# Kernel optimization log

Measured on AMD Instinct MI355X. Metric: run time of the kernel, lower is better.

Reference implementation:

```python
import jax, jax.numpy as jnp
import numpy as np

VERY_SMOL_NUM = -1e9  # undefined global in source; interpreted as large negative mask value
D_K = 128


def setup_inputs() -> dict:
    key = jax.random.key(0)
    k1, k2, k3 = jax.random.split(key, 3)
    B, S, D = 16, 2048, D_K
    Q = jax.random.normal(k1, (B, S, D), dtype=jnp.float32)
    K = jax.random.normal(k2, (B, S, D), dtype=jnp.float32)
    V = jax.random.normal(k3, (B, S, D), dtype=jnp.float32)
    return {"Q": Q, "K": K, "V": V}


def reference(Q, K, V):
    B, S, d_k = Q.shape
    # scores: [B, S, S] = Q @ K^T, scaled by 1/sqrt(d_k)
    x = jnp.einsum("bqd,bkd->bqk", Q, K) / jnp.sqrt(jnp.asarray(d_k, Q.dtype))
    # mask() is called unconditionally in the source (masked=False -> applied once):
    # add strict upper-triangular VERY_SMOL_NUM
    tri = jnp.triu(jnp.ones((S, S), dtype=x.dtype), k=1) * jnp.asarray(VERY_SMOL_NUM, x.dtype)
    x = x + tri  # broadcasts over batch, matching torch.triu on full shape
    # Softmax over dim=1 (query axis), as in the source (torch.nn.Softmax(dim=1))
    x = jax.nn.softmax(x, axis=1)
    return jnp.einsum("bqk,bkd->bqd", x, V)
```

## Files before the change

kernel.cpp:

```cpp
#include <hip/hip_runtime.h>


#define B_ 16
#define S_ 2048
#define D_ 128
#define QSCALE 0.12751744416825963f
#define NEG_BIG -1e30f
#define NCH 16
#define CHQ 128
#define PB 2162688

#define ROWW 136
#define P2RW 24

#define LDS_BARRIER()                                  \
  do {                                                 \
    asm volatile("s_waitcnt lgkmcnt(0)" ::: "memory"); \
    __builtin_amdgcn_s_barrier();                      \
  } while (0)

typedef short bf16x8 __attribute__((ext_vector_type(8)));
typedef float f32x4 __attribute__((ext_vector_type(4)));
typedef unsigned short u16x4 __attribute__((ext_vector_type(4)));
typedef unsigned int u32x2 __attribute__((ext_vector_type(2)));

#if defined(__has_builtin)
#if __has_builtin(__builtin_amdgcn_exp2f)
#define EXP2F(x) __builtin_amdgcn_exp2f(x)
#endif
#endif
#ifndef EXP2F
extern "C" __device__ float __ocml_exp2_f32(float);
#define EXP2F(x) __ocml_exp2_f32(x)
#endif

static __device__ __forceinline__ unsigned short f2bf(float f) {
  unsigned int u = __builtin_bit_cast(unsigned int, f);
  u += 0x7FFFu + ((u >> 16) & 1u);
  return (unsigned short)(u >> 16);
}

__global__ __launch_bounds__(256) void sdpa_convert(
    const float* __restrict__ Qr, const float* __restrict__ Kr,
    unsigned short* __restrict__ Qb, unsigned short* __restrict__ Kb) {
  const size_t t = (size_t)blockIdx.x * 256 + threadIdx.x;
  const float* src = blockIdx.y ? Kr : Qr;
  unsigned short* dstp = blockIdx.y ? Kb : Qb;
  const float sc = blockIdx.y ? 1.0f : QSCALE;
  f32x4 x = ((const f32x4*)src)[t];
  u16x4 o;
#pragma unroll
  for (int j = 0; j < 4; ++j) o[j] = f2bf(x[j] * sc);
  ((u16x4*)dstp)[t] = o;
}

__global__ __launch_bounds__(256, 4) void sdpa_pass1(
    const short* __restrict__ Qb, const short* __restrict__ Kb,
    float* __restrict__ lp_ws, unsigned short* __restrict__ Pt) {
  const int bid = blockIdx.x;
  int j = bid >> 4;
  int g = 0;
  while (j >= NCH - g) {
    j -= NCH - g;
    ++g;
  }
  const int ci = g + j;
  const int b = (bid & 7) + 8 * ((bid >> 3) & 1);

  __shared__ __align__(16) short Qst[2][32 * ROWW];
  const int tid = threadIdx.x;
  const int w = tid >> 6, lane = tid & 63, quad = lane >> 4, l15 = lane & 15;
  const int gg = 2 * g + (w >> 1);
  const int gb = 64 * gg;
  const int kb = gb + (w & 1) * 32;

  const size_t koff = ((size_t)b * S_ + kb + l15) * D_ + quad * 8;
  bf16x8 kh0[4], kh1[4];
#pragma unroll
  for (int c = 0; c < 4; ++c) {
    kh0[c] = *(const bf16x8*)(Kb + koff + c * 32);
    kh1[c] = *(const bf16x8*)(Kb + koff + 16 * D_ + c * 32);
  }

  const int nrp = S_ - gb;
  const size_t grp =
      (size_t)4 * ((size_t)gg * S_ - (size_t)(32 * gg) * (gg - 1));
  unsigned short* pw0 = Pt + (size_t)b * PB +
                        16 * (grp + (size_t)(2 * (w & 1)) * nrp) + quad * 4;
  unsigned short* pw1 = pw0 + (size_t)16 * nrp;

  const int sr = tid >> 3, sseg = tid & 7;
  const int q_start = CHQ * ci;

  {
    const short* sq = Qb + ((size_t)(b * S_ + q_start + sr)) * D_ + sseg * 16;
    bf16x8 h0 = *(const bf16x8*)(sq), h1 = *(const bf16x8*)(sq + 8);
    short* dst = &Qst[0][sr * ROWW + sseg * 16];
    *(bf16x8*)(dst) = h0;
    *(bf16x8*)(dst + 8) = h1;
  }
  LDS_BARRIER();

#define EMIT(q0s_, ktb_, cA_, pw_, lp_)                                       \
  do {                                                                        \
    float s0_ = cA_[0], s1_ = cA_[1], s2_ = cA_[2], s3_ = cA_[3];             \
    if ((q0s_) < (ktb_) + 16) {              \
      const int q_ = (q0s_) + l15;                                            \
      if ((ktb_) + quad * 4 + 0 > q_) s0_ = NEG_BIG;                          \
      if ((ktb_) + quad * 4 + 1 > q_) s1_ = NEG_BIG;                          \
      if ((ktb_) + quad * 4 + 2 > q_) s2_ = NEG_BIG;                          \
      if ((ktb_) + quad * 4 + 3 > q_) s3_ = NEG_BIG;                          \
    }                                                                         \
    const float e0_ = EXP2F(s0_), e1_ = EXP2F(s1_);                           \
    const float e2_ = EXP2F(s2_), e3_ = EXP2F(s3_);                           \
    lp_[0] += e0_;                                                            \
    lp_[1] += e1_;                                                            \
    lp_[2] += e2_;                                                            \
    lp_[3] += e3_;                                                            \
    unsigned int w0_, w1_;                                                    \
    asm("v_cvt_pk_bf16_f32 %0, %1, %2" : "=v"(w0_) : "v"(e0_), "v"(e1_));     \
    asm("v_cvt_pk_bf16_f32 %0, %1, %2" : "=v"(w1_) : "v"(e2_), "v"(e3_));     \
    u32x2 pk2_ = {w0_, w1_};                                                  \
    *(u32x2*)((pw_) + (size_t)((q0s_)-gb + l15) * 16) = pk2_;                 \
  } while (0)

  f32x4 lp0 = {0.f, 0.f, 0.f, 0.f}, lp1 = {0.f, 0.f, 0.f, 0.f};
#pragma unroll
  for (int it = 0; it < 4; ++it) {
    const int q0 = q_start + it * 32;
    const int cur = it & 1;
    bf16x8 h0, h1;
    if (it < 3) {
      const short* sq =
          Qb + ((size_t)(b * S_ + q0 + 32 + sr)) * D_ + sseg * 16;
      h0 = *(const bf16x8*)(sq);
      h1 = *(const bf16x8*)(sq + 8);
    }
#pragma unroll
    for (int sub = 0; sub < 2; ++sub) {
      const int q0s = q0 + sub * 16;
      if (q0s >= gb) {
        const short* rowp = &Qst[cur][(sub * 16 + l15) * ROWW + quad * 8];
        bf16x8 q0v = *(const bf16x8*)(rowp);
        bf16x8 q1v = *(const bf16x8*)(rowp + 32);
        bf16x8 q2v = *(const bf16x8*)(rowp + 64);
        bf16x8 q3v = *(const bf16x8*)(rowp + 96);
        f32x4 c0 = {0.f, 0.f, 0.f, 0.f};
        f32x4 c1 = {0.f, 0.f, 0.f, 0.f};
        c0 = __builtin_amdgcn_mfma_f32_16x16x32_bf16(kh0[0], q0v, c0, 0, 0, 0);
        c1 = __builtin_amdgcn_mfma_f32_16x16x32_bf16(kh1[0], q0v, c1, 0, 0, 0);
        c0 = __builtin_amdgcn_mfma_f32_16x16x32_bf16(kh0[1], q1v, c0, 0, 0, 0);
        c1 = __builtin_amdgcn_mfma_f32_16x16x32_bf16(kh1[1], q1v, c1, 0, 0, 0);
        c0 = __builtin_amdgcn_mfma_f32_16x16x32_bf16(kh0[2], q2v, c0, 0, 0, 0);
        c1 = __builtin_amdgcn_mfma_f32_16x16x32_bf16(kh1[2], q2v, c1, 0, 0, 0);
        c0 = __builtin_amdgcn_mfma_f32_16x16x32_bf16(kh0[3], q3v, c0, 0, 0, 0);
        c1 = __builtin_amdgcn_mfma_f32_16x16x32_bf16(kh1[3], q3v, c1, 0, 0, 0);
        EMIT(q0s, kb, c0, pw0, lp0);
        EMIT(q0s, kb + 16, c1, pw1, lp1);
      }
    }
    if (it < 3) {
      short* dst = &Qst[1 - cur][sr * ROWW + sseg * 16];
      *(bf16x8*)(dst) = h0;
      *(bf16x8*)(dst + 8) = h1;
    }
    LDS_BARRIER();
  }
#undef EMIT

#pragma unroll
  for (int d = 1; d < 16; d <<= 1) {
#pragma unroll
    for (int r = 0; r < 4; ++r) {
      lp0[r] += __shfl_xor(lp0[r], d, 64);
      lp1[r] += __shfl_xor(lp1[r], d, 64);
    }
  }
  if (l15 == 0) {
    float* dst = lp_ws + ((size_t)b * NCH + ci) * S_ + kb;
    *(f32x4*)(dst + quad * 4) = lp0;
    *(f32x4*)(dst + 16 + quad * 4) = lp1;
  }
}

__global__ __launch_bounds__(256) void sdpa_vscale(
    const float* __restrict__ Vr, const float* __restrict__ lp_ws,
    unsigned short* __restrict__ Vf) {
  __shared__ float Vld[32][132];
  __shared__ float as[32];
  const int kt = blockIdx.x, b = blockIdx.y, tid = threadIdx.x;
  const int k0 = kt * 32;
  const int row = tid >> 3, seg = tid & 7;
  const float* src = Vr + ((size_t)(b * S_ + k0 + row)) * D_ + seg * 16;
#pragma unroll
  for (int j = 0; j < 4; ++j) {
    f32x4 x = *(const f32x4*)(src + 4 * j);
    *(f32x4*)&Vld[row][seg * 16 + 4 * j] = x;
  }
  if (tid < 32) {
    const int k = k0 + tid;
    const int first = k >> 7;
    float l = 0.f;
#pragma unroll
    for (int ci = 0; ci < NCH; ++ci)
      if (ci >= first) l += lp_ws[((size_t)b * NCH + ci) * S_ + k];
    as[tid] = 1.0f / l;
  }
  __syncthreads();
  unsigned short* dst = Vf + ((size_t)(b * 64 + kt)) * 4096 + (size_t)tid * 16;
#pragma unroll
  for (int i = 0; i < 2; ++i) {
    const int u = tid * 2 + i;
    const int dt = u >> 6, l15 = (u >> 2) & 15, quad = u & 3;
    bf16x8 o;
#pragma unroll
    for (int e = 0; e < 8; ++e) {
      const int k = quad * 8 + e;
      o[e] = (short)f2bf(Vld[k][dt * 16 + l15] * as[k]);
    }
    *(bf16x8*)(dst + i * 8) = o;
  }
}

__global__ __launch_bounds__(512, 2) void sdpa_pass2(
    const unsigned short* __restrict__ Pt,
    const unsigned short* __restrict__ Vf, float* __restrict__ Out) {
  __shared__ __align__(16) short Pst[2][4 * 64 * P2RW];
  const int bid = blockIdx.x;
  const int b = (bid & 7) + 8 * ((bid >> 3) & 1);
  const int py = bid >> 4;
  const int tid = threadIdx.x;
  const int w = tid >> 6, lane = tid & 63, quad = lane >> 4, l15 = lane & 15;
  const int qh = w & 3;
  const int dh = w >> 2;

  const int sp = tid >> 7, su = tid & 127, srow = su >> 1, sh = su & 1;

  const unsigned short* Vbase = Vf + (size_t)b * (64 * 4096) +
                                (size_t)(dh * 4) * 512 + l15 * 32 + quad * 8;
  const int ard = ((quad >> 1) * 64 + 16 * qh + l15) * P2RW + (quad & 1) * 8;
  const int awr = (sp * 64 + srow) * P2RW + sh * 8;

#define VLOAD(tp_, V_)                                              \
  do {                                                              \
    const unsigned short* v0_ = Vbase + (size_t)(2 * (tp_)) * 4096; \
    _Pragma("unroll") for (int d_ = 0; d_ < 4; ++d_) {              \
      V_[d_] = *(const bf16x8*)(v0_ + d_ * 512);                    \
      V_[d_ + 4] = *(const bf16x8*)(v0_ + 4096 + d_ * 512);         \
    }                                                               \
  } while (0)

#define PLOAD(bx_, tp_, R_)                                                \
  do {                                                                     \
    const int pitch_ = 16 * (S_ - 64 * (tp_));                             \
    const unsigned short* g_ = Pt + (size_t)b * PB +                       \
                               2048 * (tp_) * (65 - (tp_)) + sp * pitch_ + \
                               (64 * ((bx_) - (tp_)) + srow) * 16 + sh * 8; \
    R_ = *(const bf16x8*)g_;                                               \
  } while (0)

#define MMAT(A0_, A1_, V_)                                                   \
  do {                                                                       \
    _Pragma("unroll") for (int d_ = 0; d_ < 4; ++d_) acc[d_] =               \
        __builtin_amdgcn_mfma_f32_16x16x32_bf16(A0_, V_[d_], acc[d_], 0, 0,  \
                                                0);                          \
    _Pragma("unroll") for (int d_ = 0; d_ < 4; ++d_) acc[d_] =               \
        __builtin_amdgcn_mfma_f32_16x16x32_bf16(A1_, V_[d_ + 4], acc[d_], 0, \
                                                0, 0);                       \
  } while (0)

#pragma unroll
  for (int ti = 0; ti < 2; ++ti) {
    const int bx = ti ? (31 - py) : py;
    const int count = bx + 1;
    f32x4 acc[4];
#pragma unroll
    for (int d = 0; d < 4; ++d) acc[d] = (f32x4){0.f, 0.f, 0.f, 0.f};

    bf16x8 vA[8], vB[8], sreg;
    __builtin_amdgcn_s_barrier();
    PLOAD(bx, 0, sreg);
    VLOAD(0, vA);
    *(bf16x8*)&Pst[0][awr] = sreg;
    LDS_BARRIER();

    int tp = 0;
    while (tp + 2 <= count) {
      VLOAD(tp + 1, vB);
      PLOAD(bx, tp + 1, sreg);
      {
        bf16x8 A0 = *(const bf16x8*)&Pst[tp & 1][ard];
        bf16x8 A1 = *(const bf16x8*)&Pst[tp & 1][ard + 2 * 64 * P2RW];
        MMAT(A0, A1, vA);
      }
      *(bf16x8*)&Pst[(tp & 1) ^ 1][awr] = sreg;
      LDS_BARRIER();
      if (tp + 2 < count) {
        VLOAD(tp + 2, vA);
        PLOAD(bx, tp + 2, sreg);
      }
      {
        bf16x8 A0 = *(const bf16x8*)&Pst[(tp & 1) ^ 1][ard];
        bf16x8 A1 = *(const bf16x8*)&Pst[(tp & 1) ^ 1][ard + 2 * 64 * P2RW];
        MMAT(A0, A1, vB);
      }
      if (tp + 2 < count) {
        *(bf16x8*)&Pst[tp & 1][awr] = sreg;
      }
      LDS_BARRIER();
      tp += 2;
    }
    if (tp < count) {
      bf16x8 A0 = *(const bf16x8*)&Pst[tp & 1][ard];
      bf16x8 A1 = *(const bf16x8*)&Pst[tp & 1][ard + 2 * 64 * P2RW];
      MMAT(A0, A1, vA);
    }

    const int qw = 64 * bx + 16 * qh;
#pragma unroll
    for (int r = 0; r < 4; ++r) {
      float* op =
          Out + ((size_t)b * S_ + qw + quad * 4 + r) * D_ + dh * 64 + l15;
#pragma unroll
      for (int d = 0; d < 4; ++d) op[d * 16] = acc[d][r];
    }
  }
#undef VLOAD
#undef PLOAD
#undef MMAT
}

extern "C" void kernel_launch(void* const* d_in, const int* in_sizes, int n_in,
                              void* d_out, int out_size, void* d_ws,
                              size_t ws_size, hipStream_t stream) {
  char* wsp = (char*)d_ws;
  float* lp_ws = (float*)wsp;
  char* p = wsp + (2 << 20);
  const size_t TSZ = (size_t)B_ * S_ * D_ * 2;
  unsigned short* Qb = (unsigned short*)(p);
  unsigned short* Kb = (unsigned short*)(p + TSZ);
  unsigned short* Vf = (unsigned short*)(p + 2 * TSZ);
  unsigned short* Pt = (unsigned short*)(p + 3 * TSZ);

  sdpa_convert<<<dim3((B_ * S_ * D_ / 4) / 256, 2), 256, 0, stream>>>(
      (const float*)d_in[0], (const float*)d_in[1], Qb, Kb);
  sdpa_pass1<<<dim3(NCH * 136), 256, 0, stream>>>(
      (const short*)Qb, (const short*)Kb, lp_ws, Pt);
  sdpa_vscale<<<dim3(S_ / 32, B_), 256, 0, stream>>>((const float*)d_in[2],
                                                     lp_ws, Vf);
  sdpa_pass2<<<dim3(256), 512, 0, stream>>>(Pt, Vf, (float*)d_out);
}
```

Measured before the change: 158.4 us.

## Stage V tiles through shared memory with a deeper register prefetch pipeline

In pass 2, V tiles were previously loaded straight from global memory into registers by each wave, so the four query-head waves sharing a d-half reloaded the same data. Now V is loaded cooperatively once per block into a double-buffered LDS array alongside P. Global loads are issued two tiles ahead, so each step prefetches P and V for tile t+3 or t+4 while computing tile t. This cuts redundant global V traffic and hides latency. The cost is 32 KB more LDS per block, which may limit occupancy at 2 blocks per CU, plus extra LDS reads and writes and more live registers.

```diff
diff --git a/kernel.cpp b/kernel.cpp
--- a/kernel.cpp
+++ b/kernel.cpp
@@ -226,6 +226,7 @@
     const unsigned short* __restrict__ Pt,
     const unsigned short* __restrict__ Vf, float* __restrict__ Out) {
   __shared__ __align__(16) short Pst[2][4 * 64 * P2RW];
+  __shared__ __align__(16) short Vst[2][8192];
   const int bid = blockIdx.x;
   const int b = (bid & 7) + 8 * ((bid >> 3) & 1);
   const int py = bid >> 4;
@@ -236,19 +237,9 @@
 
   const int sp = tid >> 7, su = tid & 127, srow = su >> 1, sh = su & 1;
 
-  const unsigned short* Vbase = Vf + (size_t)b * (64 * 4096) +
-                                (size_t)(dh * 4) * 512 + l15 * 32 + quad * 8;
   const int ard = ((quad >> 1) * 64 + 16 * qh + l15) * P2RW + (quad & 1) * 8;
   const int awr = (sp * 64 + srow) * P2RW + sh * 8;
-
-#define VLOAD(tp_, V_)                                              \
-  do {                                                              \
-    const unsigned short* v0_ = Vbase + (size_t)(2 * (tp_)) * 4096; \
-    _Pragma("unroll") for (int d_ = 0; d_ < 4; ++d_) {              \
-      V_[d_] = *(const bf16x8*)(v0_ + d_ * 512);                    \
-      V_[d_ + 4] = *(const bf16x8*)(v0_ + 4096 + d_ * 512);         \
-    }                                                               \
-  } while (0)
+  const int vrd = dh * 2048 + l15 * 32 + quad * 8;
 
 #define PLOAD(bx_, tp_, R_)                                                \
   do {                                                                     \
@@ -259,14 +250,34 @@
     R_ = *(const bf16x8*)g_;                                               \
   } while (0)
 
-#define MMAT(A0_, A1_, V_)                                                   \
+#define VSLOAD(tp_, R_)                                                    \
+  do {                                                                     \
+    const unsigned short* g_ = Vf + (size_t)b * (64 * 4096) +              \
+                               (size_t)(2 * (tp_)) * 4096 + tid * 8;       \
+    R_[0] = *(const bf16x8*)g_;                                            \
+    R_[1] = *(const bf16x8*)(g_ + 4096);                                   \
+  } while (0)
+
+#define WRITE_P(buf_, R_) *(bf16x8*)&Pst[buf_][awr] = R_
+
+#define WRITE_V(buf_, R_)                           \
+  do {                                              \
+    *(bf16x8*)&Vst[buf_][tid * 8] = R_[0];          \
+    *(bf16x8*)&Vst[buf_][4096 + tid * 8] = R_[1];   \
+  } while (0)
+
+#define COMPUTE(buf_)                                                        \
   do {                                                                       \
-    _Pragma("unroll") for (int d_ = 0; d_ < 4; ++d_) acc[d_] =               \
-        __builtin_amdgcn_mfma_f32_16x16x32_bf16(A0_, V_[d_], acc[d_], 0, 0,  \
-                                                0);                          \
-    _Pragma("unroll") for (int d_ = 0; d_ < 4; ++d_) acc[d_] =               \
-        __builtin_amdgcn_mfma_f32_16x16x32_bf16(A1_, V_[d_ + 4], acc[d_], 0, \
-                                                0, 0);                       \
+    bf16x8 A0 = *(const bf16x8*)&Pst[buf_][ard];                             \
+    bf16x8 A1 = *(const bf16x8*)&Pst[buf_][ard + 2 * 64 * P2RW];             \
+    _Pragma("unroll") for (int d_ = 0; d_ < 4; ++d_) {                       \
+      bf16x8 v0_ = *(const bf16x8*)&Vst[buf_][vrd + d_ * 512];               \
+      bf16x8 v1_ = *(const bf16x8*)&Vst[buf_][4096 + vrd + d_ * 512];        \
+      acc[d_] = __builtin_amdgcn_mfma_f32_16x16x32_bf16(A0, v0_, acc[d_],    \
+                                                        0, 0, 0);            \
+      acc[d_] = __builtin_amdgcn_mfma_f32_16x16x32_bf16(A1, v1_, acc[d_],    \
+                                                        0, 0, 0);            \
+    }                                                                        \
   } while (0)
 
 #pragma unroll
@@ -277,43 +288,51 @@
 #pragma unroll
     for (int d = 0; d < 4; ++d) acc[d] = (f32x4){0.f, 0.f, 0.f, 0.f};
 
-    bf16x8 vA[8], vB[8], sreg;
+    bf16x8 sP0, sP1, sV0[2], sV1[2];
     __builtin_amdgcn_s_barrier();
-    PLOAD(bx, 0, sreg);
-    VLOAD(0, vA);
-    *(bf16x8*)&Pst[0][awr] = sreg;
+    PLOAD(bx, 0, sP0);
+    VSLOAD(0, sV0);
+    WRITE_P(0, sP0);
+    WRITE_V(0, sV0);
+    if (count > 1) {
+      PLOAD(bx, 1, sP0);
+      VSLOAD(1, sV0);
+    }
+    if (count > 2) {
+      PLOAD(bx, 2, sP1);
+      VSLOAD(2, sV1);
+    }
     LDS_BARRIER();
 
     int tp = 0;
     while (tp + 2 <= count) {
-      VLOAD(tp + 1, vB);
-      PLOAD(bx, tp + 1, sreg);
+      const int cur = tp & 1;
       {
-        bf16x8 A0 = *(const bf16x8*)&Pst[tp & 1][ard];
-        bf16x8 A1 = *(const bf16x8*)&Pst[tp & 1][ard + 2 * 64 * P2RW];
-        MMAT(A0, A1, vA);
-      }
-      *(bf16x8*)&Pst[(tp & 1) ^ 1][awr] = sreg;
-      LDS_BARRIER();
-      if (tp + 2 < count) {
-        VLOAD(tp + 2, vA);
-        PLOAD(bx, tp + 2, sreg);
+        WRITE_P(cur ^ 1, sP0);
+        WRITE_V(cur ^ 1, sV0);
+        if (tp + 3 < count) {
+          PLOAD(bx, tp + 3, sP0);
+          VSLOAD(tp + 3, sV0);
+        }
+        COMPUTE(cur);
+        LDS_BARRIER();
       }
       {
-        bf16x8 A0 = *(const bf16x8*)&Pst[(tp & 1) ^ 1][ard];
-        bf16x8 A1 = *(const bf16x8*)&Pst[(tp & 1) ^ 1][ard + 2 * 64 * P2RW];
-        MMAT(A0, A1, vB);
+        if (tp + 2 < count) {
+          WRITE_P(cur, sP1);
+          WRITE_V(cur, sV1);
+        }
+        if (tp + 4 < count) {
+          PLOAD(bx, tp + 4, sP1);
+          VSLOAD(tp + 4, sV1);
+        }
+        COMPUTE(cur ^ 1);
+        LDS_BARRIER();
       }
-      if (tp + 2 < count) {
-        *(bf16x8*)&Pst[tp & 1][awr] = sreg;
-      }
-      LDS_BARRIER();
       tp += 2;
     }
     if (tp < count) {
-      bf16x8 A0 = *(const bf16x8*)&Pst[tp & 1][ard];
-      bf16x8 A1 = *(const bf16x8*)&Pst[tp & 1][ard + 2 * 64 * P2RW];
-      MMAT(A0, A1, vA);
+      COMPUTE(tp & 1);
     }
 
     const int qw = 64 * bx + 16 * qh;
@@ -325,9 +344,11 @@
       for (int d = 0; d < 4; ++d) op[d * 16] = acc[d][r];
     }
   }
-#undef VLOAD
 #undef PLOAD
-#undef MMAT
+#undef VSLOAD
+#undef WRITE_P
+#undef WRITE_V
+#undef COMPUTE
 }
 
 extern "C" void kernel_launch(void* const* d_in, const int* in_sizes, int n_in,
```

Measured after the change: 140.9 us. 1.12x faster.
